# Performance work log

Measured on AMD Instinct MI355X. Metric: run time of the kernel, lower is better.

The kernel has to match this reference:

```python
import jax, jax.numpy as jnp
import numpy as np

N_EMBD = 2048
N_HEAD = 16
KV_GROUP = 4
HEAD_DIM = N_EMBD // N_HEAD          # 128
N_KV = N_HEAD // KV_GROUP            # 4
KV_DIM = N_KV * HEAD_DIM             # 512
B, T = 2, 2048
ROPE_THETA = 1000000.0


def setup_inputs() -> dict:
    key = jax.random.key(0)
    k0, k1, k2 = jax.random.split(key, 3)
    x = jax.random.normal(k0, (B, T, N_EMBD), dtype=jnp.float32)
    # weights stored (in, out); matches torch Linear math up to a transpose of random init
    W_attn = jax.random.normal(k1, (N_EMBD, N_EMBD + 2 * KV_DIM), dtype=jnp.float32) * 0.02
    b_attn = jnp.zeros((N_EMBD + 2 * KV_DIM,), dtype=jnp.float32)
    W_proj = jax.random.normal(k2, (N_EMBD, N_EMBD), dtype=jnp.float32) * 0.02
    # realistic RoPE frequencies (Qwen-style theta)
    inv_freq = 1.0 / (ROPE_THETA ** (np.arange(0, HEAD_DIM, 2, dtype=np.float64) / HEAD_DIM))
    ang = np.outer(np.arange(T, dtype=np.float64), inv_freq)  # (T, HEAD_DIM//2)
    freqs_cos = jnp.asarray(np.cos(ang), dtype=jnp.float32)
    freqs_sin = jnp.asarray(np.sin(ang), dtype=jnp.float32)
    return {"x": x, "W_attn": W_attn, "b_attn": b_attn, "W_proj": W_proj,
            "freqs_cos": freqs_cos, "freqs_sin": freqs_sin}


def _rope_expand(x, cos, sin, kv_group):
    # x: (B, T, n_kv, hd); complex rotate interleaved pairs, then expand to n_kv*kv_group heads
    Bx, Tx, nh, hd = x.shape
    xf = x.astype(jnp.float32).reshape(Bx, Tx, nh, hd // 2, 2)
    a, b = xf[..., 0], xf[..., 1]
    c = cos[None, :, None, :]  # (1, T, 1, hd//2)
    s = sin[None, :, None, :]
    yr = a * c - b * s
    yi = a * s + b * c
    y = jnp.stack([yr, yi], axis=-1).reshape(Bx, Tx, nh, hd)
    y = jnp.broadcast_to(y[:, :, :, None, :], (Bx, Tx, nh, kv_group, hd))
    return y.reshape(Bx, Tx, nh * kv_group, hd).astype(x.dtype)


def reference(x, W_attn, b_attn, W_proj, freqs_cos, freqs_sin):
    Bx, Tx, E = x.shape
    hd = 2 * freqs_cos.shape[-1]
    n_q = E // hd
    kv_dim = (W_attn.shape[1] - E) // 2
    n_kv = kv_dim // hd
    g = n_q // n_kv

    qkv = x @ W_attn + b_attn  # (B, T, E + 2*kv_dim)
    q = qkv[..., :E].reshape(Bx, Tx, n_q, hd).transpose(0, 2, 1, 3)          # bhtd
    k = qkv[..., E:E + kv_dim].reshape(Bx, Tx, n_kv, hd)
    v = qkv[..., E + kv_dim:].reshape(Bx, Tx, n_kv, hd)
    # faithful to source: RoPE on K AND V (not Q), then GQA expand
    k = _rope_expand(k, freqs_cos, freqs_sin, g).transpose(0, 2, 1, 3)       # bhtd
    v = _rope_expand(v, freqs_cos, freqs_sin, g).transpose(0, 2, 1, 3)       # bhtd

    scale = 1.0 / jnp.sqrt(jnp.asarray(hd, dtype=x.dtype))
    scores = jnp.einsum('bhqd,bhkd->bhqk', q, k) * scale                     # (B, H, T, T)
    causal = jnp.tril(jnp.ones((Tx, Tx), dtype=bool))
    scores = jnp.where(causal, scores, jnp.asarray(-jnp.inf, scores.dtype))
    attn = jax.nn.softmax(scores, axis=-1)
    y = jnp.einsum('bhqk,bhkd->bhqd', attn, v)
    y = y.transpose(0, 2, 1, 3).reshape(Bx, Tx, E)
    return y @ W_proj  # c_proj, no bias
```

## Files before the change

kernel.cpp:

```cpp
#include <hip/hip_runtime.h>
#include <cstdint>
#include <cstddef>

#define T_SEQ 2048
#define B_SZ  2
#define EMB   2048
#define NH    16
#define NKV   4
#define HD    128
#define KVD   512
#define QKVN  3072
#define MROWS (B_SZ*T_SEQ)

typedef __bf16 bf16x8 __attribute__((ext_vector_type(8)));
typedef float  f32x4  __attribute__((ext_vector_type(4)));
typedef short  s16x8  __attribute__((ext_vector_type(8)));
typedef unsigned short u16;

__device__ __forceinline__ u16 f2b(float f) {
  uint32_t u = __builtin_bit_cast(uint32_t, f);
  u += 0x7fffu + ((u >> 16) & 1u);
  return (u16)(u >> 16);
}
__device__ __forceinline__ float b2f(u16 h) {
  return __builtin_bit_cast(float, (uint32_t)h << 16);
}
__device__ __forceinline__ bf16x8 ld_bf8(const u16* p) {
  return __builtin_bit_cast(bf16x8, *(const s16x8*)p);
}
__device__ __forceinline__ void glds16(const void* g, void* l) {
  __builtin_amdgcn_global_load_lds((const __attribute__((address_space(1))) void*)g,
                                   (__attribute__((address_space(3))) void*)l, 16, 0, 0);
}
template<int N> __device__ __forceinline__ void waitv() {
  if constexpr (N == 0) asm volatile("s_waitcnt vmcnt(0)" ::: "memory");
  else if constexpr (N == 2) asm volatile("s_waitcnt vmcnt(2)" ::: "memory");
  else if constexpr (N == 3) asm volatile("s_waitcnt vmcnt(3)" ::: "memory");
  __builtin_amdgcn_sched_barrier(0);
}

__global__ void cvt_x_kernel(const float4* __restrict__ x, ushort4* __restrict__ xb, int n4) {
  int i = blockIdx.x*blockDim.x + threadIdx.x;
  if (i >= n4) return;
  float4 v = x[i];
  ushort4 o;
  o.x = f2b(v.x); o.y = f2b(v.y); o.z = f2b(v.z); o.w = f2b(v.w);
  xb[i] = o;
}

__global__ void transpose_w_kernel(const float* __restrict__ in, u16* __restrict__ out,
                                   int R, int C) {
  __shared__ float tile[32][33];
  int c0 = blockIdx.x*32, r0 = blockIdx.y*32;
  int tx = threadIdx.x, ty = threadIdx.y;
#pragma unroll
  for (int i = 0; i < 32; i += 8)
    tile[ty+i][tx] = in[(size_t)(r0+ty+i)*C + c0+tx];
  __syncthreads();
#pragma unroll
  for (int i = 0; i < 32; i += 8)
    out[(size_t)(c0+ty+i)*R + r0+tx] = f2b(tile[tx][ty+i]);
}

template<int BN, int WGN, int MF, int NF, int NF1, int SB, int SB1, int VMC, bool BF16_OUT>
__global__ __launch_bounds__(512, 2) void gemm_kernel(const u16* __restrict__ A,
        const u16* __restrict__ Bt, const float* __restrict__ bias,
        void* __restrict__ Cout, int M, int N, int K) {
  constexpr int MF2 = MF/2;
  __shared__ u16 As[2][256*64];
  __shared__ u16 Bs[2][BN*64];
  const int tid = threadIdx.x;
  const int w = tid >> 6, lane = tid & 63;
  const int quad = lane >> 4, lc = lane & 15;
  const int wrow = w / WGN, wcol = w % WGN;
  const int gx = gridDim.x;
  const int lin = blockIdx.y*gx + blockIdx.x;
  const int swz = (lin & 7)*32 + (lin >> 3);
  const int m0 = (swz / gx)*256, n0 = (swz % gx)*BN;

  f32x4 acc[MF][NF] = {};
  bf16x8 af[MF2][2], bfv[NF][2];

  int xoff[2];
#pragma unroll
  for (int ks = 0; ks < 2; ++ks) xoff[ks] = ((ks*4 + quad) ^ (lc & 7))*8;
  const int arow0 = (wrow*MF*16 + lc)*64;
  const int brow0 = (wcol*NF*16 + lc)*64;

  const int srb  = tid >> 3;
  const int spos = (tid & 7) ^ (srb & 7);
  const u16* sAp = A  + (size_t)(m0 + srb)*K + spos*8;
  const u16* sBp = Bt + (size_t)(n0 + srb)*K + spos*8;

#define STAGE_A(bf_, t_, h_) do { \
    glds16(sAp + (size_t)((h_)*2  )*64*K + (size_t)(t_)*64, &As[bf_][((h_)*2  )*4096 + w*512]); \
    glds16(sAp + (size_t)((h_)*2+1)*64*K + (size_t)(t_)*64, &As[bf_][((h_)*2+1)*4096 + w*512]); \
  } while (0)
#define STAGE_B(bf_, t_, p_) do { \
    _Pragma("unroll") for (int r = (p_) ? SB1 : 0; r < ((p_) ? SB : SB1); ++r) \
      glds16(sBp + (size_t)r*64*K + (size_t)(t_)*64, &Bs[bf_][r*4096 + w*512]); \
  } while (0)
#define LDAH(S_, h_) do { _Pragma("unroll") for (int i = 0; i < MF2; ++i) { \
    af[i][0] = ld_bf8((S_) + arow0 + ((h_)*MF2 + i)*1024 + xoff[0]); \
    af[i][1] = ld_bf8((S_) + arow0 + ((h_)*MF2 + i)*1024 + xoff[1]); } } while (0)
#define LDBG(S_, g_) do { _Pragma("unroll") for (int j = (g_) ? NF1 : 0; j < ((g_) ? NF : NF1); ++j) { \
    bfv[j][0] = ld_bf8((S_) + brow0 + j*1024 + xoff[0]); \
    bfv[j][1] = ld_bf8((S_) + brow0 + j*1024 + xoff[1]); } } while (0)
#define CL(h_, g_) do { _Pragma("unroll") for (int ks = 0; ks < 2; ++ks) \
    _Pragma("unroll") for (int i = 0; i < MF2; ++i) \
    _Pragma("unroll") for (int j = (g_) ? NF1 : 0; j < ((g_) ? NF : NF1); ++j) \
      acc[(h_)*MF2+i][j] = __builtin_amdgcn_mfma_f32_16x16x32_bf16( \
          af[i][ks], bfv[j][ks], acc[(h_)*MF2+i][j], 0, 0, 0); } while (0)
#define BARX()  __builtin_amdgcn_s_barrier()
#define SCHB()  __builtin_amdgcn_sched_barrier(0)
#define MFMAPH(h_, g_) do { BARX(); \
    asm volatile("s_waitcnt lgkmcnt(0)" ::: "memory"); SCHB(); \
    __builtin_amdgcn_s_setprio(1); CL(h_, g_); __builtin_amdgcn_s_setprio(0); \
  } while (0)

  const int NT = K >> 6;
  STAGE_B(0, 0, 0); STAGE_B(0, 0, 1);
  STAGE_A(0, 0, 0); STAGE_A(0, 0, 1);
  STAGE_B(1, 1, 0); STAGE_B(1, 1, 1);
  waitv<VMC>();
  BARX(); SCHB();

  for (int t0 = 0; t0 < NT-2; t0 += 2) {
    const u16 *a0 = As[0], *b0 = Bs[0], *a1 = As[1], *b1 = Bs[1];
    LDAH(a0, 0); LDBG(b0, 0); STAGE_A(1, t0+1, 0);
    MFMAPH(0, 0); BARX();
    LDBG(b0, 1); STAGE_A(1, t0+1, 1);
    MFMAPH(0, 1); BARX();
    LDAH(a0, 1); STAGE_B(0, t0+2, 0);
    MFMAPH(1, 0); BARX();
    STAGE_B(0, t0+2, 1);
    MFMAPH(1, 1);
    waitv<VMC>();
    BARX(); SCHB();
    LDAH(a1, 0); LDBG(b1, 0); STAGE_A(0, t0+2, 0);
    MFMAPH(0, 0); BARX();
    LDBG(b1, 1); STAGE_A(0, t0+2, 1);
    MFMAPH(0, 1); BARX();
    LDAH(a1, 1); STAGE_B(1, t0+3, 0);
    MFMAPH(1, 0); BARX();
    STAGE_B(1, t0+3, 1);
    MFMAPH(1, 1);
    waitv<VMC>();
    BARX(); SCHB();
  }
  {
    const u16 *a0 = As[0], *b0 = Bs[0], *a1 = As[1], *b1 = Bs[1];
    LDAH(a0, 0); LDBG(b0, 0); STAGE_A(1, NT-1, 0);
    MFMAPH(0, 0); BARX();
    LDBG(b0, 1); STAGE_A(1, NT-1, 1);
    MFMAPH(0, 1); BARX();
    LDAH(a0, 1);
    MFMAPH(1, 0); BARX();
    MFMAPH(1, 1);
    waitv<0>();
    BARX(); SCHB();
    LDAH(a1, 0); LDBG(b1, 0);
    MFMAPH(0, 0); BARX();
    LDBG(b1, 1);
    MFMAPH(0, 1); BARX();
    LDAH(a1, 1);
    MFMAPH(1, 0); BARX();
    MFMAPH(1, 1);
  }

#undef STAGE_A
#undef STAGE_B
#undef LDAH
#undef LDBG
#undef CL
#undef BARX
#undef SCHB
#undef MFMAPH

#pragma unroll
  for (int j = 0; j < NF; ++j) {
    int col = n0 + wcol*NF*16 + j*16 + lc;
    float bv = BF16_OUT ? bias[col] : 0.0f;
#pragma unroll
    for (int i = 0; i < MF; ++i) {
      int rowb = m0 + wrow*MF*16 + i*16 + quad*4;
#pragma unroll
      for (int r = 0; r < 4; ++r) {
        float v = acc[i][j][r] + bv;
        if (BF16_OUT) ((u16*)Cout)[(size_t)(rowb+r)*N + col] = f2b(v);
        else          ((float*)Cout)[(size_t)(rowb+r)*N + col] = v;
      }
    }
  }
}

__global__ void rope_kernel(const u16* __restrict__ qkv, const float* __restrict__ fc,
                            const float* __restrict__ fs, u16* __restrict__ kout,
                            u16* __restrict__ vout) {
  int tid = threadIdx.x;
  int row = blockIdx.x;
  int i = tid & 63, kv = tid >> 6;
  int t = row & (T_SEQ-1);
  const u16* p = qkv + (size_t)row*QKVN + EMB + kv*HD + 2*i;
  float ka = b2f(p[0]),   kb = b2f(p[1]);
  float va = b2f(p[KVD]), vb = b2f(p[KVD+1]);
  float c = fc[t*64+i], s = fs[t*64+i];
  size_t ob = (size_t)row*KVD + kv*HD + 2*i;
  kout[ob]   = f2b(ka*c - kb*s);
  kout[ob+1] = f2b(ka*s + kb*c);
  vout[ob]   = f2b(va*c - vb*s);
  vout[ob+1] = f2b(va*s + vb*c);
}

__global__ void transpose_v_kernel(const u16* __restrict__ vb, u16* __restrict__ vtb) {
  __shared__ u16 tile[32][33];
  int bkv = blockIdx.z;
  int b = bkv >> 2, kv = bkv & 3;
  int d0 = blockIdx.y*32, t0 = blockIdx.x*32;
  int tx = threadIdx.x, ty = threadIdx.y;
#pragma unroll
  for (int i = 0; i < 32; i += 8)
    tile[ty+i][tx] = vb[(size_t)(b*T_SEQ + t0+ty+i)*KVD + kv*HD + d0 + tx];
  __syncthreads();
#pragma unroll
  for (int i = 0; i < 32; i += 8)
    vtb[(size_t)(bkv*HD + d0+ty+i)*T_SEQ + t0 + tx] = tile[tx][ty+i];
}

__global__ __launch_bounds__(256, 2) void flash_kernel(const u16* __restrict__ qkv,
    const u16* __restrict__ kb, const u16* __restrict__ vtb, u16* __restrict__ yb) {
  constexpr int PP = 72;
  __shared__ u16 Ks[2][64*128];
  __shared__ u16 Vs[2][128*64];
  __shared__ u16 Ps[4][16*PP];
  const int tid = threadIdx.x;
  const int w = tid >> 6, lane = tid & 63;
  const int quad = lane >> 4, lc = lane & 15;
  const int bkv = blockIdx.x & 7;
  const int r_  = blockIdx.x >> 3;
  const int b = bkv >> 2, kv = bkv & 3;
  const int h = kv*4 + w;
  const int qbase = (127 - r_)*16;

  bf16x8 qf[4];
  {
    const u16* qp = qkv + (size_t)(b*T_SEQ + qbase + lc)*QKVN + h*HD + quad*8;
#pragma unroll
    for (int ks = 0; ks < 4; ++ks) qf[ks] = ld_bf8(qp + ks*32);
  }

  f32x4 o[8] = {};
  float rs[4] = {0.f, 0.f, 0.f, 0.f};
  const u16* kbase = kb  + (size_t)b*T_SEQ*KVD + kv*HD;
  const u16* vbase = vtb + (size_t)bkv*HD*T_SEQ;
  const int nk = qbase + 16;
  const int nt = (nk + 63) >> 6;
  const float cs = 0.08838834764831845f * 1.4426950408889634f;
  u16* pw = Ps[w];

  const u16* kptr[4];
  const u16* vptr[4];
#pragma unroll
  for (int rr = 0; rr < 4; ++rr) {
    int krow = (rr*4 + w)*4 + (lane >> 4);
    int kcc  = (lane & 15) ^ (krow & 15);
    kptr[rr] = kbase + (size_t)krow*KVD + kcc*8;
    int vrow = (rr*4 + w)*8 + (lane >> 3);
    int vcc  = (lane & 7) ^ (vrow & 7);
    vptr[rr] = vbase + (size_t)vrow*T_SEQ + vcc*8;
  }

  int koff[4], voff[2];
#pragma unroll
  for (int ks = 0; ks < 4; ++ks) koff[ks] = lc*128 + (((ks*4 + quad) ^ lc)*8);
#pragma unroll
  for (int ks = 0; ks < 2; ++ks) voff[ks] = lc*64 + (((ks*4 + quad) ^ (lc & 7))*8);

#pragma unroll
  for (int rr = 0; rr < 4; ++rr) glds16(kptr[rr], &Ks[0][(rr*4 + w)*512]);
#pragma unroll
  for (int rr = 0; rr < 4; ++rr) glds16(vptr[rr], &Vs[0][(rr*4 + w)*512]);
  asm volatile("s_waitcnt vmcnt(0)" ::: "memory");
  __builtin_amdgcn_sched_barrier(0);
  __builtin_amdgcn_s_barrier();
  __builtin_amdgcn_sched_barrier(0);

  for (int t = 0; t < nt; ++t) {
    const int cur = t & 1;
    if (t + 1 < nt) {
#pragma unroll
      for (int rr = 0; rr < 4; ++rr)
        glds16(kptr[rr] + (size_t)(t+1)*64*KVD, &Ks[cur^1][(rr*4 + w)*512]);
#pragma unroll
      for (int rr = 0; rr < 4; ++rr)
        glds16(vptr[rr] + (size_t)(t+1)*64,     &Vs[cur^1][(rr*4 + w)*512]);
    }
    const u16* ksb = Ks[cur];
    const u16* vsb = Vs[cur];
    const int k0 = t*64;

    f32x4 sc[4] = {};
    __builtin_amdgcn_s_setprio(1);
#pragma unroll
    for (int nt2 = 0; nt2 < 4; ++nt2)
#pragma unroll
      for (int ks = 0; ks < 4; ++ks) {
        bf16x8 kf = ld_bf8(ksb + nt2*16*128 + koff[ks]);
        sc[nt2] = __builtin_amdgcn_mfma_f32_16x16x32_bf16(qf[ks], kf, sc[nt2], 0, 0, 0);
      }
    __builtin_amdgcn_s_setprio(0);

    if (k0 + 63 > qbase) {
#pragma unroll
      for (int nt2 = 0; nt2 < 4; ++nt2) {
        int key = k0 + nt2*16 + lc;
        int qrow = qbase + quad*4;
#pragma unroll
        for (int r = 0; r < 4; ++r) {
          float e = __builtin_amdgcn_exp2f(sc[nt2][r]*cs);
          float p = (key <= qrow + r) ? e : 0.0f;
          rs[r] += p;
          pw[(quad*4 + r)*PP + nt2*16 + lc] = f2b(p);
        }
      }
    } else {
#pragma unroll
      for (int nt2 = 0; nt2 < 4; ++nt2)
#pragma unroll
        for (int r = 0; r < 4; ++r) {
          float p = __builtin_amdgcn_exp2f(sc[nt2][r]*cs);
          rs[r] += p;
          pw[(quad*4 + r)*PP + nt2*16 + lc] = f2b(p);
        }
    }

    bf16x8 pa[2];
#pragma unroll
    for (int ks = 0; ks < 2; ++ks)
      pa[ks] = ld_bf8(pw + lc*PP + ks*32 + quad*8);

    __builtin_amdgcn_s_setprio(1);
#pragma unroll
    for (int j = 0; j < 8; ++j)
#pragma unroll
      for (int ks = 0; ks < 2; ++ks) {
        bf16x8 vf = ld_bf8(vsb + j*16*64 + voff[ks]);
        o[j] = __builtin_amdgcn_mfma_f32_16x16x32_bf16(pa[ks], vf, o[j], 0, 0, 0);
      }
    __builtin_amdgcn_s_setprio(0);

    asm volatile("s_waitcnt vmcnt(0)" ::: "memory");
    __builtin_amdgcn_sched_barrier(0);
    __builtin_amdgcn_s_barrier();
    __builtin_amdgcn_sched_barrier(0);
  }

#pragma unroll
  for (int r = 0; r < 4; ++r) {
    float v = rs[r];
#pragma unroll
    for (int off2 = 8; off2 >= 1; off2 >>= 1)
      v += __shfl_xor(v, off2);
    float inv = 1.0f / v;
    size_t orow = (size_t)(b*T_SEQ + qbase + quad*4 + r)*EMB + h*HD;
#pragma unroll
    for (int j = 0; j < 8; ++j)
      yb[orow + j*16 + lc] = f2b(o[j][r]*inv);
  }
}

extern "C" void kernel_launch(void* const* d_in, const int* in_sizes, int n_in,
                              void* d_out, int out_size, void* d_ws, size_t ws_size,
                              hipStream_t stream) {
  const float* x      = (const float*)d_in[0];
  const float* W_attn = (const float*)d_in[1];
  const float* b_attn = (const float*)d_in[2];
  const float* W_proj = (const float*)d_in[3];
  const float* fc     = (const float*)d_in[4];
  const float* fs     = (const float*)d_in[5];

  u16* ws   = (u16*)d_ws;
  u16* xb   = ws;
  u16* WaT  = xb   + (size_t)MROWS*EMB;
  u16* qkv  = WaT  + (size_t)QKVN*EMB;
  u16* kbuf = qkv  + (size_t)MROWS*QKVN;
  u16* vb   = kbuf + (size_t)MROWS*KVD;
  u16* vtb  = vb   + (size_t)MROWS*KVD;
  u16* WpT  = WaT;
  u16* yb   = xb;
  float* out = (float*)d_out;

  cvt_x_kernel<<<(MROWS*EMB/4 + 255)/256, 256, 0, stream>>>(
      (const float4*)x, (ushort4*)xb, MROWS*EMB/4);
  transpose_w_kernel<<<dim3(QKVN/32, EMB/32), dim3(32, 8), 0, stream>>>(
      W_attn, WaT, EMB, QKVN);
  gemm_kernel<192, 4, 8, 3, 2, 3, 2, 3, true>
      <<<dim3(QKVN/192, MROWS/256), 512, 0, stream>>>(
      xb, WaT, b_attn, qkv, MROWS, QKVN, EMB);
  rope_kernel<<<MROWS, 256, 0, stream>>>(qkv, fc, fs, kbuf, vb);
  transpose_v_kernel<<<dim3(T_SEQ/32, HD/32, B_SZ*NKV), dim3(32, 8), 0, stream>>>(vb, vtb);
  transpose_w_kernel<<<dim3(EMB/32, EMB/32), dim3(32, 8), 0, stream>>>(
      W_proj, WpT, EMB, EMB);
  flash_kernel<<<dim3(B_SZ*NKV*(T_SEQ/16)), 256, 0, stream>>>(qkv, kbuf, vtb, yb);
  gemm_kernel<128, 2, 4, 4, 2, 2, 1, 2, false>
      <<<dim3(EMB/128, MROWS/256), 512, 0, stream>>>(
      yb, WpT, nullptr, out, MROWS, EMB, EMB);
}
```

Baseline: 281.4 us.

## Process two query tiles per flash block to share K/V LDS tiles

Flash attention blocks grow to 512 threads (8 waves) handling two 16-row query tiles per head group, so each K/V tile loaded into LDS serves twice the query rows and global loads per wave are halved. The P scratch buffer switches from padded rows to an XOR-swizzled layout. This adds some redundant masked work for the lower query tile, and the tighter launch bounds may force register spills and reduce occupancy.

```diff
diff --git a/kernel.cpp b/kernel.cpp
--- a/kernel.cpp
+++ b/kernel.cpp
@@ -227,20 +227,21 @@
     vtb[(size_t)(bkv*HD + d0+ty+i)*T_SEQ + t0 + tx] = tile[tx][ty+i];
 }
 
-__global__ __launch_bounds__(256, 2) void flash_kernel(const u16* __restrict__ qkv,
+__global__ __launch_bounds__(512, 4) void flash_kernel(const u16* __restrict__ qkv,
     const u16* __restrict__ kb, const u16* __restrict__ vtb, u16* __restrict__ yb) {
-  constexpr int PP = 72;
   __shared__ u16 Ks[2][64*128];
   __shared__ u16 Vs[2][128*64];
-  __shared__ u16 Ps[4][16*PP];
+  __shared__ u16 Ps[8][16*64];
   const int tid = threadIdx.x;
   const int w = tid >> 6, lane = tid & 63;
   const int quad = lane >> 4, lc = lane & 15;
   const int bkv = blockIdx.x & 7;
   const int r_  = blockIdx.x >> 3;
   const int b = bkv >> 2, kv = bkv & 3;
-  const int h = kv*4 + w;
-  const int qbase = (127 - r_)*16;
+  const int h  = kv*4 + (w & 3);
+  const int qt = w >> 2;
+  const int qbaseB = (63 - r_)*32;
+  const int qbase  = qbaseB + qt*16;
 
   bf16x8 qf[4];
   {
@@ -253,33 +254,41 @@
   float rs[4] = {0.f, 0.f, 0.f, 0.f};
   const u16* kbase = kb  + (size_t)b*T_SEQ*KVD + kv*HD;
   const u16* vbase = vtb + (size_t)bkv*HD*T_SEQ;
-  const int nk = qbase + 16;
+  const int nk = qbaseB + 32;
   const int nt = (nk + 63) >> 6;
   const float cs = 0.08838834764831845f * 1.4426950408889634f;
   u16* pw = Ps[w];
 
-  const u16* kptr[4];
-  const u16* vptr[4];
-#pragma unroll
-  for (int rr = 0; rr < 4; ++rr) {
-    int krow = (rr*4 + w)*4 + (lane >> 4);
-    int kcc  = (lane & 15) ^ (krow & 15);
+  const u16* kptr[2];
+  const u16* vptr[2];
+#pragma unroll
+  for (int rr = 0; rr < 2; ++rr) {
+    int ci = rr*512 + w*64 + lane;
+    int krow = ci >> 4, kcc = (ci & 15) ^ (krow & 15);
     kptr[rr] = kbase + (size_t)krow*KVD + kcc*8;
-    int vrow = (rr*4 + w)*8 + (lane >> 3);
-    int vcc  = (lane & 7) ^ (vrow & 7);
+    int vrow = ci >> 3, vcc = (ci & 7) ^ (vrow & 7);
     vptr[rr] = vbase + (size_t)vrow*T_SEQ + vcc*8;
   }
 
-  int koff[4], voff[2];
+  int koff[4], voff[2], poff[2];
 #pragma unroll
   for (int ks = 0; ks < 4; ++ks) koff[ks] = lc*128 + (((ks*4 + quad) ^ lc)*8);
 #pragma unroll
   for (int ks = 0; ks < 2; ++ks) voff[ks] = lc*64 + (((ks*4 + quad) ^ (lc & 7))*8);
-
-#pragma unroll
-  for (int rr = 0; rr < 4; ++rr) glds16(kptr[rr], &Ks[0][(rr*4 + w)*512]);
-#pragma unroll
-  for (int rr = 0; rr < 4; ++rr) glds16(vptr[rr], &Vs[0][(rr*4 + w)*512]);
+#pragma unroll
+  for (int ks = 0; ks < 2; ++ks) poff[ks] = lc*64 + (((ks*4 + quad) ^ (lc & 7))*8);
+  int pwb[4], pwx[4];
+#pragma unroll
+  for (int r = 0; r < 4; ++r) {
+    pwb[r] = (quad*4 + r)*64 + (lc & 7);
+    pwx[r] = (quad*4 + r) & 7;
+  }
+  const int pcc = lc >> 3;
+
+#pragma unroll
+  for (int rr = 0; rr < 2; ++rr) glds16(kptr[rr], &Ks[0][rr*4096 + w*512]);
+#pragma unroll
+  for (int rr = 0; rr < 2; ++rr) glds16(vptr[rr], &Vs[0][rr*4096 + w*512]);
   asm volatile("s_waitcnt vmcnt(0)" ::: "memory");
   __builtin_amdgcn_sched_barrier(0);
   __builtin_amdgcn_s_barrier();
@@ -289,11 +298,11 @@
     const int cur = t & 1;
     if (t + 1 < nt) {
 #pragma unroll
-      for (int rr = 0; rr < 4; ++rr)
-        glds16(kptr[rr] + (size_t)(t+1)*64*KVD, &Ks[cur^1][(rr*4 + w)*512]);
-#pragma unroll
-      for (int rr = 0; rr < 4; ++rr)
-        glds16(vptr[rr] + (size_t)(t+1)*64,     &Vs[cur^1][(rr*4 + w)*512]);
+      for (int rr = 0; rr < 2; ++rr)
+        glds16(kptr[rr] + (size_t)(t+1)*64*KVD, &Ks[cur^1][rr*4096 + w*512]);
+#pragma unroll
+      for (int rr = 0; rr < 2; ++rr)
+        glds16(vptr[rr] + (size_t)(t+1)*64,     &Vs[cur^1][rr*4096 + w*512]);
     }
     const u16* ksb = Ks[cur];
     const u16* vsb = Vs[cur];
@@ -320,7 +329,7 @@
           float e = __builtin_amdgcn_exp2f(sc[nt2][r]*cs);
           float p = (key <= qrow + r) ? e : 0.0f;
           rs[r] += p;
-          pw[(quad*4 + r)*PP + nt2*16 + lc] = f2b(p);
+          pw[pwb[r] + ((nt2*2 + pcc) ^ pwx[r])*8] = f2b(p);
         }
       }
     } else {
@@ -330,14 +339,14 @@
         for (int r = 0; r < 4; ++r) {
           float p = __builtin_amdgcn_exp2f(sc[nt2][r]*cs);
           rs[r] += p;
-          pw[(quad*4 + r)*PP + nt2*16 + lc] = f2b(p);
+          pw[pwb[r] + ((nt2*2 + pcc) ^ pwx[r])*8] = f2b(p);
         }
     }
 
     bf16x8 pa[2];
 #pragma unroll
     for (int ks = 0; ks < 2; ++ks)
-      pa[ks] = ld_bf8(pw + lc*PP + ks*32 + quad*8);
+      pa[ks] = ld_bf8(pw + poff[ks]);
 
     __builtin_amdgcn_s_setprio(1);
 #pragma unroll
@@ -401,7 +410,7 @@
   transpose_v_kernel<<<dim3(T_SEQ/32, HD/32, B_SZ*NKV), dim3(32, 8), 0, stream>>>(vb, vtb);
   transpose_w_kernel<<<dim3(EMB/32, EMB/32), dim3(32, 8), 0, stream>>>(
       W_proj, WpT, EMB, EMB);
-  flash_kernel<<<dim3(B_SZ*NKV*(T_SEQ/16)), 256, 0, stream>>>(qkv, kbuf, vtb, yb);
+  flash_kernel<<<dim3(B_SZ*NKV*(T_SEQ/32)), 512, 0, stream>>>(qkv, kbuf, vtb, yb);
   gemm_kernel<128, 2, 4, 4, 2, 2, 1, 2, false>
       <<<dim3(EMB/128, MROWS/256), 512, 0, stream>>>(
       yb, WpT, nullptr, out, MROWS, EMB, EMB);
```

After: 286.9 us. No clear change (+2.0%).
